# Kernel optimization log

Measured on AMD Instinct MI355X. Metric: run time of the kernel, lower is better.

## Reference

```python
import jax, jax.numpy as jnp
import numpy as np

THETA = 0.5  # forward default arg
ALPHA = 0.2  # LeakyReLU negative slope
NEG_INF = -9e15


def setup_inputs() -> dict:
    key = jax.random.key(0)
    k1, k2, k3, k4, k5 = jax.random.split(key, 5)
    N, F_IN, F_OUT = 8192, 256, 256
    h = jax.random.normal(k1, (N, F_IN), dtype=jnp.float32)
    adj = jax.random.randint(k2, (N, N), 0, 2, dtype=jnp.int32)
    cv_values = jax.random.uniform(k3, (N,), dtype=jnp.float32)
    # xavier_uniform with gain=1.414
    g = 1.414
    bw = g * np.sqrt(6.0 / (F_IN + F_OUT))
    W = jax.random.uniform(k4, (F_IN, F_OUT), dtype=jnp.float32, minval=-bw, maxval=bw)
    ba = g * np.sqrt(6.0 / (2 * F_OUT + 1))
    a = jax.random.uniform(k5, (2 * F_OUT, 1), dtype=jnp.float32, minval=-ba, maxval=ba)
    return {"h": h, "adj": adj, "cv_values": cv_values, "W": W, "a": a}


def reference(h, adj, cv_values, W, a):
    # Wh: [N, F_out]
    Wh = h @ W
    F_out = Wh.shape[1]
    a1 = a[:F_out, 0]   # [F_out]
    a2 = a[F_out:, 0]   # [F_out]
    # e_ij = LeakyReLU([Wh_i ; Wh_j] . a) = LeakyReLU(Wh_i.a1 + Wh_j.a2)
    f1 = Wh @ a1        # [N]
    f2 = Wh @ a2        # [N]
    e = jax.nn.leaky_relu(f1[:, None] + f2[None, :], negative_slope=ALPHA)
    # CV bias: theta * cv_i broadcast across row i
    e = e + THETA * cv_values[:, None]
    att = jnp.where(adj > 0, e, jnp.float32(NEG_INF))
    att = jax.nn.softmax(att, axis=1)
    # dropout is identity in eval mode (training=False)
    h_prime = att @ Wh  # [N, F_out]
    return jax.nn.elu(h_prime)  # concat=True branch
```

## Files before the change

### kernel.cpp

```cpp
#include <hip/hip_runtime.h>
#include <cstdint>
#include <cstddef>

typedef _Float16 half8 __attribute__((ext_vector_type(8)));
typedef _Float16 half4 __attribute__((ext_vector_type(4)));
typedef float f32x4 __attribute__((ext_vector_type(4)));

#define GAT_N 8192
#define GAT_F 256
#define GAT_NW 256
#define GAT_ALPHA 0.2f
#define GAT_LOG2E 1.4426950408889634f

__device__ inline unsigned enc_f32(float x) {
    unsigned b = __float_as_uint(x);
    return (b & 0x80000000u) ? ~b : (b | 0x80000000u);
}
__device__ inline float dec_f32(unsigned u) {
    unsigned b = (u & 0x80000000u) ? (u ^ 0x80000000u) : ~u;
    return __uint_as_float(b);
}

__global__ __launch_bounds__(256) void gat_k0_pack(
    const int* __restrict__ adj, unsigned char* __restrict__ adjB)
{
    const int wv = threadIdx.x >> 6;
    const int lane = threadIdx.x & 63;
    const int row = blockIdx.x * 4 + wv;
    const int* src = adj + (size_t)row * GAT_N;
    unsigned char* dst = adjB + (size_t)row * (GAT_N / 8);
    #pragma unroll 4
    for (int k = 0; k < 16; ++k) {
        const int4 v0 = *reinterpret_cast<const int4*>(src + k * 512 + lane * 8);
        const int4 v1 = *reinterpret_cast<const int4*>(src + k * 512 + lane * 8 + 4);
        unsigned m = (unsigned)(v0.x > 0)        | ((unsigned)(v0.y > 0) << 1)
                   | ((unsigned)(v0.z > 0) << 2) | ((unsigned)(v0.w > 0) << 3)
                   | ((unsigned)(v1.x > 0) << 4) | ((unsigned)(v1.y > 0) << 5)
                   | ((unsigned)(v1.z > 0) << 6) | ((unsigned)(v1.w > 0) << 7);
        dst[k * 64 + lane] = (unsigned char)m;
    }
}

__global__ __launch_bounds__(256) void gat_k0b_convert(
    const float* __restrict__ W, _Float16* __restrict__ WT,
    unsigned* __restrict__ f2mxEnc)
{
    const int g = blockIdx.x * 256 + threadIdx.x;
    if (g == 0) *f2mxEnc = 0u;
    const int k = g >> 8, n = g & 255;
    WT[n * GAT_F + k] = (_Float16)W[g];
}

__global__ __launch_bounds__(256, 2) void gat_k1_gemm(
    const float* __restrict__ h, const _Float16* __restrict__ WT,
    const float* __restrict__ a, _Float16* __restrict__ whT,
    float* __restrict__ f1L, float* __restrict__ f2L,
    unsigned* __restrict__ f2mxEnc)
{
    __shared__ float sP1[4][16], sP2[4][16];
    const int wv = threadIdx.x >> 6;
    const int lane = threadIdx.x & 63;
    const int l15 = lane & 15;
    const int quad = lane >> 4;
    const int r0 = blockIdx.x * 16;

    f32x4 acc[4];
    #pragma unroll
    for (int t = 0; t < 4; ++t) { f32x4 z = {0.f,0.f,0.f,0.f}; acc[t] = z; }

    #pragma unroll
    for (int k0 = 0; k0 < GAT_F; k0 += 32) {
        const float* ap = h + (size_t)(r0 + l15) * GAT_F + k0 + quad * 8;
        const float4 a0 = *reinterpret_cast<const float4*>(ap);
        const float4 a1 = *reinterpret_cast<const float4*>(ap + 4);
        half8 af;
        af[0] = (_Float16)a0.x; af[1] = (_Float16)a0.y;
        af[2] = (_Float16)a0.z; af[3] = (_Float16)a0.w;
        af[4] = (_Float16)a1.x; af[5] = (_Float16)a1.y;
        af[6] = (_Float16)a1.z; af[7] = (_Float16)a1.w;
        #pragma unroll
        for (int t = 0; t < 4; ++t) {
            half8 bf = *reinterpret_cast<const half8*>(
                WT + (size_t)(wv * 64 + t * 16 + l15) * GAT_F + k0 + quad * 8);
            acc[t] = __builtin_amdgcn_mfma_f32_16x16x32_f16(af, bf, acc[t], 0, 0, 0);
        }
    }

    float p1[4] = {0.f,0.f,0.f,0.f}, p2[4] = {0.f,0.f,0.f,0.f};
    #pragma unroll
    for (int t = 0; t < 4; ++t) {
        float a1c = a[wv * 64 + t * 16 + l15];
        float a2c = a[GAT_F + wv * 64 + t * 16 + l15];
        #pragma unroll
        for (int r = 0; r < 4; ++r) {
            p1[r] = fmaf(acc[t][r], a1c, p1[r]);
            p2[r] = fmaf(acc[t][r], a2c, p2[r]);
        }
    }
    #pragma unroll
    for (int off = 1; off < 16; off <<= 1) {
        #pragma unroll
        for (int r = 0; r < 4; ++r) {
            p1[r] += __shfl_xor(p1[r], off);
            p2[r] += __shfl_xor(p2[r], off);
        }
    }
    if (l15 == 0) {
        #pragma unroll
        for (int r = 0; r < 4; ++r) {
            sP1[wv][quad * 4 + r] = p1[r];
            sP2[wv][quad * 4 + r] = p2[r];
        }
    }
    __syncthreads();
    if (threadIdx.x < 16) {
        const int row = threadIdx.x;
        const float s1 = (sP1[0][row] + sP1[1][row] + sP1[2][row] + sP1[3][row]) * GAT_LOG2E;
        const float s2 = (sP2[0][row] + sP2[1][row] + sP2[2][row] + sP2[3][row]) * GAT_LOG2E;
        f1L[r0 + row] = s1;
        f2L[r0 + row] = s2;
        float mx = s2;
        #pragma unroll
        for (int off = 1; off < 16; off <<= 1) mx = fmaxf(mx, __shfl_xor(mx, off));
        if (row == 0) atomicMax(f2mxEnc, enc_f32(mx));
    }

    #pragma unroll
    for (int t = 0; t < 4; ++t) {
        half4 hv;
        #pragma unroll
        for (int r = 0; r < 4; ++r) hv[r] = (_Float16)acc[t][r];
        *reinterpret_cast<half4*>(
            whT + (size_t)(wv * 64 + t * 16 + l15) * GAT_N + r0 + quad * 4) = hv;
    }
}

__global__ __launch_bounds__(256, 3) void gat_k3_attn(
    const unsigned* __restrict__ adjW, const float* __restrict__ f1L,
    const float* __restrict__ f2L, const unsigned* __restrict__ f2mxEnc,
    const _Float16* __restrict__ whT,
    _Float16* __restrict__ Ph,
    float* __restrict__ L)
{
    __shared__ __align__(16) _Float16 sB[2][8192];

    const int bx = blockIdx.x;
    const int q  = bx & 7;
    const int fh = (bx >> 3) & 1;
    const int rb = bx >> 4;
    const int wv = threadIdx.x >> 6;
    const int lane = threadIdx.x & 63;
    const int l15 = lane & 15;
    const int quad = lane >> 4;

    const int r0 = rb * 128 + wv * 32;
    const int rA = r0 + l15;
    const int rB = rA + 16;

    const float fmxL = dec_f32(*f2mxEnc);
    const float f1A = f1L[rA];
    const float f1B = f1L[rB];
    const float sA = f1A + fmxL;
    const float sBv = f1B + fmxL;
    const float CA = fmaxf(sA, GAT_ALPHA * sA);
    const float CB = fmaxf(sBv, GAT_ALPHA * sBv);

    f32x4 acc[2][8];
    #pragma unroll
    for (int s = 0; s < 2; ++s)
        #pragma unroll
        for (int t = 0; t < 8; ++t) {
            f32x4 z = {0.f,0.f,0.f,0.f};
            acc[s][t] = z;
        }
    float d0 = 0.f, d1 = 0.f;

    const int kq = q * 1024;
    const uint2* awA = reinterpret_cast<const uint2*>(adjW + (size_t)rA * GAT_NW + q * 32);
    const uint2* awB = reinterpret_cast<const uint2*>(adjW + (size_t)rB * GAT_NW + q * 32);
    const float* f2q = f2L + kq + quad * 8;

    const _Float16* gst = whT + (size_t)(fh * 128 + lane) * GAT_N + kq + wv * 8;

    #define STAGE(buf, step)                                                   \
        {                                                                      \
            _Pragma("unroll")                                                  \
            for (int i = 0; i < 4; ++i) {                                      \
                const _Float16* gp = gst + (size_t)((i & 1) * 64) * GAT_N      \
                                     + (i >> 1) * 32 + (step) * 64;            \
                _Float16* lp = &sB[buf][((wv + (i >> 1) * 4) * 128             \
                                         + (i & 1) * 64) * 8];                 \
                __builtin_amdgcn_global_load_lds(                              \
                    (const __attribute__((address_space(1))) void*)gp,         \
                    (__attribute__((address_space(3))) void*)lp, 16, 0, 0);    \
            }                                                                  \
        }

    uint2 nA = awA[0];
    uint2 nB = awB[0];
    float4 nfa = *reinterpret_cast<const float4*>(f2q);
    float4 nfb = *reinterpret_cast<const float4*>(f2q + 4);
    STAGE(0, 0)
    __syncthreads();

    for (int step = 0; step < 16; ++step) {
        const int cur = step & 1;
        const uint2 cA = nA, cB = nB;
        if (step < 15) {
            nA = awA[step + 1];
            nB = awB[step + 1];
            STAGE(1 - cur, step + 1)
        }

        #pragma unroll
        for (int k2 = 0; k2 < 2; ++k2) {
            const int u = step * 2 + k2;
            const float4 cfa = nfa, cfb = nfb;
            if (u < 31) {
                nfa = *reinterpret_cast<const float4*>(f2q + (u + 1) * 32);
                nfb = *reinterpret_cast<const float4*>(f2q + (u + 1) * 32 + 4);
            }
            const unsigned wA = k2 ? cA.y : cA.x;
            const unsigned wB = k2 ? cB.y : cB.x;
            const unsigned mA = (wA >> (quad * 8)) & 0xffu;
            const unsigned mB = (wB >> (quad * 8)) & 0xffu;
            const float f2v[8] = {cfa.x, cfa.y, cfa.z, cfa.w,
                                  cfb.x, cfb.y, cfb.z, cfb.w};

            half8 pA, pB;
            #pragma unroll
            for (int j = 0; j < 8; ++j) {
                const float f2j = f2v[j];
                float xa = f1A + f2j;
                float la = fmaxf(xa, GAT_ALPHA * xa);
                float pa = __builtin_amdgcn_exp2f(la - CA);
                pa = (mA & (1u << j)) ? pa : 0.f;
                d0 += pa;
                pA[j] = (_Float16)pa;
                float xb = f1B + f2j;
                float lb = fmaxf(xb, GAT_ALPHA * xb);
                float pb = __builtin_amdgcn_exp2f(lb - CB);
                pb = (mB & (1u << j)) ? pb : 0.f;
                d1 += pb;
                pB[j] = (_Float16)pb;
            }

            const int lbase = (k2 * 4 + quad) * 1024 + l15 * 8;
            #pragma unroll
            for (int t = 0; t < 8; ++t) {
                half8 bf = *reinterpret_cast<const half8*>(
                    &sB[cur][lbase + t * 128]);
                acc[0][t] = __builtin_amdgcn_mfma_f32_16x16x32_f16(pA, bf, acc[0][t], 0, 0, 0);
                acc[1][t] = __builtin_amdgcn_mfma_f32_16x16x32_f16(pB, bf, acc[1][t], 0, 0, 0);
            }
        }
        __syncthreads();
    }
    #undef STAGE

    d0 += __shfl_xor(d0, 16); d0 += __shfl_xor(d0, 32);
    d1 += __shfl_xor(d1, 16); d1 += __shfl_xor(d1, 32);
    if (fh == 0 && lane < 16) {
        float* Lq = L + q * GAT_N;
        Lq[rA] = d0; Lq[rB] = d1;
    }

    const int wid = rb * 4 + wv;
    _Float16* Pq = Ph + ((size_t)q * 256 + wid) * 8192;
    #pragma unroll
    for (int s = 0; s < 2; ++s)
        #pragma unroll
        for (int t = 0; t < 8; ++t) {
            const int tt = fh * 8 + t;
            half4 hv;
            #pragma unroll
            for (int r = 0; r < 4; ++r) hv[r] = (_Float16)acc[s][t][r];
            *reinterpret_cast<half4*>(Pq + (size_t)(((s * 16 + tt) * 64 + lane) * 4)) = hv;
        }
}

__global__ __launch_bounds__(256) void gat_k4_final(
    const _Float16* __restrict__ Ph, const float* __restrict__ L,
    float* __restrict__ out)
{
    const int tid = threadIdx.x;
    const int wid = blockIdx.x >> 3;
    __shared__ float s_rl[32];
    if (tid < 32) {
        const int row = wid * 32 + tid;
        float s = 0.f;
        #pragma unroll
        for (int q = 0; q < 8; ++q) s += L[q * GAT_N + row];
        s_rl[tid] = 1.0f / fmaxf(s, 1e-30f);
    }
    __syncthreads();

    const int idx = blockIdx.x * 256 + tid;
    const int rem = idx & 2047;
    const int lane = rem & 63;
    const int st = rem >> 6;
    const int s = st >> 4, t = st & 15;
    const int l15 = lane & 15, quad = lane >> 4;
    const int lrow0 = s * 16 + quad * 4;
    const int col = t * 16 + l15;

    float accv[4] = {0.f, 0.f, 0.f, 0.f};
    #pragma unroll
    for (int q = 0; q < 8; ++q) {
        half4 v = *reinterpret_cast<const half4*>(
            Ph + ((size_t)q * 256 + wid) * 8192 + (size_t)rem * 4);
        #pragma unroll
        for (int r = 0; r < 4; ++r) accv[r] += (float)v[r];
    }
    #pragma unroll
    for (int r = 0; r < 4; ++r) {
        const float v = accv[r] * s_rl[lrow0 + r];
        const float o = v > 0.f ? v : expm1f(v);
        out[(size_t)(wid * 32 + lrow0 + r) * GAT_F + col] = o;
    }
}

extern "C" void kernel_launch(void* const* d_in, const int* in_sizes, int n_in,
                              void* d_out, int out_size, void* d_ws, size_t ws_size,
                              hipStream_t stream)
{
    const float* h   = (const float*)d_in[0];
    const int*   adj = (const int*)d_in[1];
    const float* W   = (const float*)d_in[3];
    const float* a   = (const float*)d_in[4];
    float* out = (float*)d_out;
    char* ws = (char*)d_ws;

    const size_t SLAB = (size_t)GAT_N * GAT_F * 2;

    size_t off = 0;
    _Float16* whT = (_Float16*)(ws + off); off += SLAB;
    _Float16* Ph  = (_Float16*)(ws + off); off += 8 * SLAB;
    unsigned char* adjB = (unsigned char*)(ws + off); off += (size_t)GAT_N * GAT_N / 8;
    _Float16* WT  = (_Float16*)(ws + off); off += (size_t)GAT_F * GAT_F * 2;
    float* f1L = (float*)(ws + off); off += GAT_N * 4;
    float* f2L = (float*)(ws + off); off += GAT_N * 4;
    float* L   = (float*)(ws + off); off += 8 * GAT_N * 4;
    unsigned* f2mxEnc = (unsigned*)(ws + off); off += 256;

    gat_k0_pack<<<2048, 256, 0, stream>>>(adj, adjB);
    gat_k0b_convert<<<256, 256, 0, stream>>>(W, WT, f2mxEnc);
    gat_k1_gemm<<<512, 256, 0, stream>>>(h, WT, a, whT, f1L, f2L, f2mxEnc);
    gat_k3_attn<<<1024, 256, 0, stream>>>((const unsigned*)adjB, f1L, f2L, f2mxEnc, whT, Ph, L);
    gat_k4_final<<<2048, 256, 0, stream>>>(Ph, L, out);
}
```

Baseline: 466.5 us.

## Factor softmax exponentials into per-column tables and double rows per wave

Precomputes per-column exp2 tables E and E5, computed once with the global max of f2. The per-element LeakyReLU+exp becomes a compare and a multiply against per-row constants. Each wave now handles 64 rows instead of 32, which reuses each staged B tile across twice as many MFMAs and halves the grid. In exchange it needs more accumulator registers (occupancy hint lowered to 2) and adds a small kernel, with possible range and precision issues in the factored exponentials.

```diff
diff --git a/kernel.cpp b/kernel.cpp
--- a/kernel.cpp
+++ b/kernel.cpp
@@ -135,9 +135,20 @@
     }
 }
 
-__global__ __launch_bounds__(256, 3) void gat_k3_attn(
+__global__ __launch_bounds__(256) void gat_k2e_tables(
+    const float* __restrict__ f2L, const unsigned* __restrict__ f2mxEnc,
+    float* __restrict__ E, float* __restrict__ E5)
+{
+    const int i = blockIdx.x * 256 + threadIdx.x;
+    const float d = f2L[i] - dec_f32(*f2mxEnc);
+    E[i]  = __builtin_amdgcn_exp2f(d);
+    E5[i] = __builtin_amdgcn_exp2f(GAT_ALPHA * d);
+}
+
+__global__ __launch_bounds__(256, 2) void gat_k3_attn(
     const unsigned* __restrict__ adjW, const float* __restrict__ f1L,
-    const float* __restrict__ f2L, const unsigned* __restrict__ f2mxEnc,
+    const unsigned* __restrict__ f2mxEnc,
+    const float* __restrict__ E, const float* __restrict__ E5,
     const _Float16* __restrict__ whT,
     _Float16* __restrict__ Ph,
     float* __restrict__ L)
@@ -153,35 +164,38 @@
     const int l15 = lane & 15;
     const int quad = lane >> 4;
 
-    const int r0 = rb * 128 + wv * 32;
-    const int rA = r0 + l15;
-    const int rB = rA + 16;
+    const int r0 = rb * 256 + wv * 64;
 
     const float fmxL = dec_f32(*f2mxEnc);
-    const float f1A = f1L[rA];
-    const float f1B = f1L[rB];
-    const float sA = f1A + fmxL;
-    const float sBv = f1B + fmxL;
-    const float CA = fmaxf(sA, GAT_ALPHA * sA);
-    const float CB = fmaxf(sBv, GAT_ALPHA * sBv);
-
-    f32x4 acc[2][8];
-    #pragma unroll
-    for (int s = 0; s < 2; ++s)
+    float Tc[4], Kc[4], Mc[4];
+    #pragma unroll
+    for (int s = 0; s < 4; ++s) {
+        const float sA = f1L[r0 + s * 16 + l15] + fmxL;
+        const float C = fmaxf(sA, GAT_ALPHA * sA);
+        Tc[s] = __builtin_amdgcn_exp2f(-sA);
+        Kc[s] = __builtin_amdgcn_exp2f(sA - C);
+        Mc[s] = __builtin_amdgcn_exp2f(GAT_ALPHA * sA - C);
+    }
+
+    f32x4 acc[4][8];
+    #pragma unroll
+    for (int s = 0; s < 4; ++s)
         #pragma unroll
         for (int t = 0; t < 8; ++t) {
             f32x4 z = {0.f,0.f,0.f,0.f};
             acc[s][t] = z;
         }
-    float d0 = 0.f, d1 = 0.f;
+    float dsum[4] = {0.f, 0.f, 0.f, 0.f};
 
     const int kq = q * 1024;
-    const uint2* awA = reinterpret_cast<const uint2*>(adjW + (size_t)rA * GAT_NW + q * 32);
-    const uint2* awB = reinterpret_cast<const uint2*>(adjW + (size_t)rB * GAT_NW + q * 32);
-    const float* f2q = f2L + kq + quad * 8;
+    const uint2* aw0 = reinterpret_cast<const uint2*>(adjW + (size_t)(r0 + 0*16 + l15) * GAT_NW + q * 32);
+    const uint2* aw1 = reinterpret_cast<const uint2*>(adjW + (size_t)(r0 + 1*16 + l15) * GAT_NW + q * 32);
+    const uint2* aw2 = reinterpret_cast<const uint2*>(adjW + (size_t)(r0 + 2*16 + l15) * GAT_NW + q * 32);
+    const uint2* aw3 = reinterpret_cast<const uint2*>(adjW + (size_t)(r0 + 3*16 + l15) * GAT_NW + q * 32);
+    const float* Eq  = E  + kq + quad * 8;
+    const float* E5q = E5 + kq + quad * 8;
 
     const _Float16* gst = whT + (size_t)(fh * 128 + lane) * GAT_N + kq + wv * 8;
-
     #define STAGE(buf, step)                                                   \
         {                                                                      \
             _Pragma("unroll")                                                  \
@@ -196,53 +210,57 @@
             }                                                                  \
         }
 
-    uint2 nA = awA[0];
-    uint2 nB = awB[0];
-    float4 nfa = *reinterpret_cast<const float4*>(f2q);
-    float4 nfb = *reinterpret_cast<const float4*>(f2q + 4);
+    uint2 n0 = aw0[0], n1 = aw1[0], n2 = aw2[0], n3 = aw3[0];
+    float4 nEa = *reinterpret_cast<const float4*>(Eq);
+    float4 nEb = *reinterpret_cast<const float4*>(Eq + 4);
+    float4 nFa = *reinterpret_cast<const float4*>(E5q);
+    float4 nFb = *reinterpret_cast<const float4*>(E5q + 4);
     STAGE(0, 0)
     __syncthreads();
 
     for (int step = 0; step < 16; ++step) {
         const int cur = step & 1;
-        const uint2 cA = nA, cB = nB;
+        const uint2 c0 = n0, c1 = n1, c2 = n2, c3 = n3;
         if (step < 15) {
-            nA = awA[step + 1];
-            nB = awB[step + 1];
+            n0 = aw0[step + 1]; n1 = aw1[step + 1];
+            n2 = aw2[step + 1]; n3 = aw3[step + 1];
             STAGE(1 - cur, step + 1)
         }
 
         #pragma unroll
         for (int k2 = 0; k2 < 2; ++k2) {
             const int u = step * 2 + k2;
-            const float4 cfa = nfa, cfb = nfb;
+            const float4 cEa = nEa, cEb = nEb, cFa = nFa, cFb = nFb;
             if (u < 31) {
-                nfa = *reinterpret_cast<const float4*>(f2q + (u + 1) * 32);
-                nfb = *reinterpret_cast<const float4*>(f2q + (u + 1) * 32 + 4);
+                nEa = *reinterpret_cast<const float4*>(Eq + (u + 1) * 32);
+                nEb = *reinterpret_cast<const float4*>(Eq + (u + 1) * 32 + 4);
+                nFa = *reinterpret_cast<const float4*>(E5q + (u + 1) * 32);
+                nFb = *reinterpret_cast<const float4*>(E5q + (u + 1) * 32 + 4);
             }
-            const unsigned wA = k2 ? cA.y : cA.x;
-            const unsigned wB = k2 ? cB.y : cB.x;
-            const unsigned mA = (wA >> (quad * 8)) & 0xffu;
-            const unsigned mB = (wB >> (quad * 8)) & 0xffu;
-            const float f2v[8] = {cfa.x, cfa.y, cfa.z, cfa.w,
-                                  cfb.x, cfb.y, cfb.z, cfb.w};
-
-            half8 pA, pB;
+            const unsigned m0 = ((k2 ? c0.y : c0.x) >> (quad * 8)) & 0xffu;
+            const unsigned m1 = ((k2 ? c1.y : c1.x) >> (quad * 8)) & 0xffu;
+            const unsigned m2 = ((k2 ? c2.y : c2.x) >> (quad * 8)) & 0xffu;
+            const unsigned m3 = ((k2 ? c3.y : c3.x) >> (quad * 8)) & 0xffu;
+            const float ev[8]  = {cEa.x, cEa.y, cEa.z, cEa.w, cEb.x, cEb.y, cEb.z, cEb.w};
+            const float fv[8]  = {cFa.x, cFa.y, cFa.z, cFa.w, cFb.x, cFb.y, cFb.z, cFb.w};
+
+            half8 p0, p1, p2, p3;
             #pragma unroll
             for (int j = 0; j < 8; ++j) {
-                const float f2j = f2v[j];
-                float xa = f1A + f2j;
-                float la = fmaxf(xa, GAT_ALPHA * xa);
-                float pa = __builtin_amdgcn_exp2f(la - CA);
-                pa = (mA & (1u << j)) ? pa : 0.f;
-                d0 += pa;
-                pA[j] = (_Float16)pa;
-                float xb = f1B + f2j;
-                float lb = fmaxf(xb, GAT_ALPHA * xb);
-                float pb = __builtin_amdgcn_exp2f(lb - CB);
-                pb = (mB & (1u << j)) ? pb : 0.f;
-                d1 += pb;
-                pB[j] = (_Float16)pb;
+                const float e = ev[j], f = fv[j];
+                float v;
+                v = (e >= Tc[0]) ? e * Kc[0] : f * Mc[0];
+                v = (m0 & (1u << j)) ? v : 0.f;
+                dsum[0] += v; p0[j] = (_Float16)v;
+                v = (e >= Tc[1]) ? e * Kc[1] : f * Mc[1];
+                v = (m1 & (1u << j)) ? v : 0.f;
+                dsum[1] += v; p1[j] = (_Float16)v;
+                v = (e >= Tc[2]) ? e * Kc[2] : f * Mc[2];
+                v = (m2 & (1u << j)) ? v : 0.f;
+                dsum[2] += v; p2[j] = (_Float16)v;
+                v = (e >= Tc[3]) ? e * Kc[3] : f * Mc[3];
+                v = (m3 & (1u << j)) ? v : 0.f;
+                dsum[3] += v; p3[j] = (_Float16)v;
             }
 
             const int lbase = (k2 * 4 + quad) * 1024 + l15 * 8;
@@ -250,32 +268,37 @@
             for (int t = 0; t < 8; ++t) {
                 half8 bf = *reinterpret_cast<const half8*>(
                     &sB[cur][lbase + t * 128]);
-                acc[0][t] = __builtin_amdgcn_mfma_f32_16x16x32_f16(pA, bf, acc[0][t], 0, 0, 0);
-                acc[1][t] = __builtin_amdgcn_mfma_f32_16x16x32_f16(pB, bf, acc[1][t], 0, 0, 0);
+                acc[0][t] = __builtin_amdgcn_mfma_f32_16x16x32_f16(p0, bf, acc[0][t], 0, 0, 0);
+                acc[1][t] = __builtin_amdgcn_mfma_f32_16x16x32_f16(p1, bf, acc[1][t], 0, 0, 0);
+                acc[2][t] = __builtin_amdgcn_mfma_f32_16x16x32_f16(p2, bf, acc[2][t], 0, 0, 0);
+                acc[3][t] = __builtin_amdgcn_mfma_f32_16x16x32_f16(p3, bf, acc[3][t], 0, 0, 0);
             }
         }
         __syncthreads();
     }
     #undef STAGE
 
-    d0 += __shfl_xor(d0, 16); d0 += __shfl_xor(d0, 32);
-    d1 += __shfl_xor(d1, 16); d1 += __shfl_xor(d1, 32);
+    #pragma unroll
+    for (int s = 0; s < 4; ++s) {
+        dsum[s] += __shfl_xor(dsum[s], 16);
+        dsum[s] += __shfl_xor(dsum[s], 32);
+    }
     if (fh == 0 && lane < 16) {
         float* Lq = L + q * GAT_N;
-        Lq[rA] = d0; Lq[rB] = d1;
+        #pragma unroll
+        for (int s = 0; s < 4; ++s) Lq[r0 + s * 16 + l15] = dsum[s];
     }
 
     const int wid = rb * 4 + wv;
-    _Float16* Pq = Ph + ((size_t)q * 256 + wid) * 8192;
-    #pragma unroll
-    for (int s = 0; s < 2; ++s)
+    _Float16* Pq = Ph + ((size_t)(q * 128 + wid) * 16384) + fh * 8192;
+    #pragma unroll
+    for (int s = 0; s < 4; ++s)
         #pragma unroll
         for (int t = 0; t < 8; ++t) {
-            const int tt = fh * 8 + t;
             half4 hv;
             #pragma unroll
             for (int r = 0; r < 4; ++r) hv[r] = (_Float16)acc[s][t][r];
-            *reinterpret_cast<half4*>(Pq + (size_t)(((s * 16 + tt) * 64 + lane) * 4)) = hv;
+            *reinterpret_cast<half4*>(Pq + (size_t)(((s * 8 + t) * 64 + lane) * 4)) = hv;
         }
 }
 
@@ -284,10 +307,10 @@
     float* __restrict__ out)
 {
     const int tid = threadIdx.x;
-    const int wid = blockIdx.x >> 3;
-    __shared__ float s_rl[32];
-    if (tid < 32) {
-        const int row = wid * 32 + tid;
+    const int wid = blockIdx.x >> 4;
+    __shared__ float s_rl[64];
+    if (tid < 64) {
+        const int row = wid * 64 + tid;
         float s = 0.f;
         #pragma unroll
         for (int q = 0; q < 8; ++q) s += L[q * GAT_N + row];
@@ -296,19 +319,21 @@
     __syncthreads();
 
     const int idx = blockIdx.x * 256 + tid;
-    const int rem = idx & 2047;
-    const int lane = rem & 63;
-    const int st = rem >> 6;
-    const int s = st >> 4, t = st & 15;
+    const int rem = idx & 4095;
+    const int fh = rem >> 11;
+    const int r2 = rem & 2047;
+    const int st = r2 >> 6;
+    const int s = st >> 3, t = st & 7;
+    const int lane = r2 & 63;
     const int l15 = lane & 15, quad = lane >> 4;
     const int lrow0 = s * 16 + quad * 4;
-    const int col = t * 16 + l15;
+    const int col = fh * 128 + t * 16 + l15;
 
     float accv[4] = {0.f, 0.f, 0.f, 0.f};
     #pragma unroll
     for (int q = 0; q < 8; ++q) {
         half4 v = *reinterpret_cast<const half4*>(
-            Ph + ((size_t)q * 256 + wid) * 8192 + (size_t)rem * 4);
+            Ph + ((size_t)(q * 128 + wid) * 16384) + fh * 8192 + (size_t)r2 * 4);
         #pragma unroll
         for (int r = 0; r < 4; ++r) accv[r] += (float)v[r];
     }
@@ -316,7 +341,7 @@
     for (int r = 0; r < 4; ++r) {
         const float v = accv[r] * s_rl[lrow0 + r];
         const float o = v > 0.f ? v : expm1f(v);
-        out[(size_t)(wid * 32 + lrow0 + r) * GAT_F + col] = o;
+        out[(size_t)(wid * 64 + lrow0 + r) * GAT_F + col] = o;
     }
 }
 
@@ -340,12 +365,16 @@
     _Float16* WT  = (_Float16*)(ws + off); off += (size_t)GAT_F * GAT_F * 2;
     float* f1L = (float*)(ws + off); off += GAT_N * 4;
     float* f2L = (float*)(ws + off); off += GAT_N * 4;
+    float* Etb = (float*)(ws + off); off += GAT_N * 4;
+    float* E5tb = (float*)(ws + off); off += GAT_N * 4;
     float* L   = (float*)(ws + off); off += 8 * GAT_N * 4;
     unsigned* f2mxEnc = (unsigned*)(ws + off); off += 256;
 
     gat_k0_pack<<<2048, 256, 0, stream>>>(adj, adjB);
     gat_k0b_convert<<<256, 256, 0, stream>>>(W, WT, f2mxEnc);
     gat_k1_gemm<<<512, 256, 0, stream>>>(h, WT, a, whT, f1L, f2L, f2mxEnc);
-    gat_k3_attn<<<1024, 256, 0, stream>>>((const unsigned*)adjB, f1L, f2L, f2mxEnc, whT, Ph, L);
+    gat_k2e_tables<<<32, 256, 0, stream>>>(f2L, f2mxEnc, Etb, E5tb);
+    gat_k3_attn<<<512, 256, 0, stream>>>((const unsigned*)adjB, f1L, f2mxEnc,
+                                         Etb, E5tb, whT, Ph, L);
     gat_k4_final<<<2048, 256, 0, stream>>>(Ph, L, out);
 }
```

After: 478.7 us. 2.6% more time.
